# Performance work log

Hardware: AMD Instinct MI355X
Metric: run time of the kernel (lower is better)

Reference implementation:

```python
import jax, jax.numpy as jnp
import numpy as np

N_VERTS = 100000
N_JOINTS = 24
N_BETAS = 10
N_POSEDIRS = 207  # (24-1)*9
# Standard SMPL kinematic tree parents
PARENTS = np.array([-1, 0, 0, 0, 1, 2, 3, 4, 5, 6, 7, 8, 9, 9, 9, 12, 13, 14, 16, 17, 18, 19, 20, 21])


def setup_inputs() -> dict:
    key = jax.random.key(0)
    ks = jax.random.split(key, 9)
    f = jnp.float32
    return {
        "betas": jax.random.normal(ks[0], (N_BETAS,), f),
        "pose": jax.random.normal(ks[1], (N_JOINTS, 3), f) * 0.2,
        "scale": jnp.ones((1,), f),
        "trans": jax.random.normal(ks[2], (3,), f),
        "v_template": jax.random.normal(ks[3], (N_VERTS, 3), f),
        "shapedirs": jax.random.normal(ks[4], (N_VERTS, 3, N_BETAS), f) * 0.01,
        "posedirs": jax.random.normal(ks[5], (N_VERTS, 3, N_POSEDIRS), f) * 0.01,
        "J_regressor": jax.random.uniform(ks[6], (N_JOINTS, N_VERTS), f) / N_VERTS,
        "weights": jax.nn.softmax(jax.random.normal(ks[7], (N_VERTS, N_JOINTS), f), axis=-1),
    }


def rodrigues(r):
    """Axis-angle [J,3] -> rotation matrices [J,3,3] (matches torch impl; eps kept tiny+deterministic)."""
    theta = jnp.linalg.norm(r + 1e-8, axis=-1, keepdims=True)  # [J,1]
    r_hat = r / theta
    z = jnp.zeros_like(r_hat[:, 0])
    K = jnp.stack([z, -r_hat[:, 2], r_hat[:, 1],
                   r_hat[:, 2], z, -r_hat[:, 0],
                   -r_hat[:, 1], r_hat[:, 0], z], axis=1).reshape(-1, 3, 3)
    c = jnp.cos(theta)[..., None]  # [J,1,1]
    s = jnp.sin(theta)[..., None]
    outer = r_hat[:, :, None] * r_hat[:, None, :]  # [J,3,3]
    I = jnp.eye(3, dtype=r.dtype)
    return c * I + (1.0 - c) * outer + s * K


def reference(betas, pose, scale, trans, v_template, shapedirs, posedirs, J_regressor, weights):
    dt = v_template.dtype
    # blend shapes
    v_shaped = jnp.einsum('vks,s->vk', shapedirs, betas) + v_template  # [V,3]
    J = J_regressor @ v_shaped  # [24,3]
    R = rodrigues(pose)  # [24,3,3]
    I3 = jnp.eye(3, dtype=dt)
    lrotmin = (R[1:] - I3).reshape(-1)  # [207]
    v_posed = v_shaped + jnp.einsum('vkp,p->vk', posedirs, lrotmin)  # [V,3]
    # forward kinematics over 24-joint chain
    bottom = jnp.array([[0.0, 0.0, 0.0, 1.0]], dtype=dt)
    def make_A(Ri, t):
        return jnp.concatenate([jnp.concatenate([Ri, t[:, None]], axis=1), bottom], axis=0)  # [4,4]
    As = [make_A(R[0], J[0])]
    for i in range(1, N_JOINTS):
        p = int(PARENTS[i])
        As.append(As[p] @ make_A(R[i], J[i] - J[p]))
    G = jnp.stack(As)  # [24,4,4]
    # remove rest-pose joint locations
    Jh = jnp.concatenate([J, jnp.zeros((N_JOINTS, 1), dt)], axis=1)  # [24,4]
    corr = jnp.einsum('jab,jb->ja', G, Jh)  # [24,4]
    rel = G - jnp.concatenate([jnp.zeros((N_JOINTS, 4, 3), dt), corr[:, :, None]], axis=2)
    # linear blend skinning
    T = jnp.einsum('vj,jab->vab', weights, rel)  # [V,4,4]
    vh = jnp.concatenate([v_posed, jnp.ones((v_posed.shape[0], 1), dt)], axis=1)  # [V,4]
    v = jnp.einsum('vab,vb->va', T, vh)[:, :3]  # [V,3]
    return v * scale.reshape(()) + trans[None, :]
```

## Files before the change

kernel.cpp:

```cpp
#include <hip/hip_runtime.h>

#define NV 100000
#define NJ 24
#define NP 207
#define NPART 25
#define VPB 8
#define NTILES (NV / VPB)
#define TF4 1242
#define GRIDF 1024

__global__ __launch_bounds__(256) void k_shape(
    const float* __restrict__ betas, const float* __restrict__ v_template,
    const float* __restrict__ shapedirs, float* __restrict__ v_shaped) {
  __shared__ float sb[10];
  if (threadIdx.x < 10) sb[threadIdx.x] = betas[threadIdx.x];
  __syncthreads();
  int R = blockIdx.x * 256 + threadIdx.x;
  if (R >= 3 * NV) return;
  const float2* sd = (const float2*)(shapedirs + (size_t)R * 10);
  float a = v_template[R];
  #pragma unroll
  for (int s = 0; s < 5; ++s) {
    float2 x = sd[s];
    a += x.x * sb[2 * s] + x.y * sb[2 * s + 1];
  }
  v_shaped[R] = a;
}

__global__ __launch_bounds__(256) void k_jreg(
    const float* __restrict__ Jreg, const float* __restrict__ v_shaped,
    float* __restrict__ jpart) {
  int j = blockIdx.x, part = blockIdx.y, tid = threadIdx.x;
  const int SL = NV / NPART;
  int v0 = part * SL;
  const float4* w4 = (const float4*)(Jreg + (size_t)j * NV + v0);
  const float4* s4 = (const float4*)(v_shaped + (size_t)3 * v0);
  float s0 = 0.f, s1 = 0.f, s2 = 0.f;
  for (int i4 = tid; i4 < SL / 4; i4 += 256) {
    float4 w = w4[i4];
    float4 A = s4[3 * i4 + 0];
    float4 B = s4[3 * i4 + 1];
    float4 C = s4[3 * i4 + 2];
    s0 += w.x * A.x + w.y * A.w + w.z * B.z + w.w * C.y;
    s1 += w.x * A.y + w.y * B.x + w.z * B.w + w.w * C.z;
    s2 += w.x * A.z + w.y * B.y + w.z * C.x + w.w * C.w;
  }
  __shared__ float red[256][3];
  red[tid][0] = s0; red[tid][1] = s1; red[tid][2] = s2;
  __syncthreads();
  for (int off = 128; off > 0; off >>= 1) {
    if (tid < off) {
      red[tid][0] += red[tid + off][0];
      red[tid][1] += red[tid + off][1];
      red[tid][2] += red[tid + off][2];
    }
    __syncthreads();
  }
  if (tid < 3) jpart[(part * NJ + j) * 3 + tid] = red[0][tid];
}

__global__ __launch_bounds__(64) void k_fk(
    const float* __restrict__ pose, const float* __restrict__ jpart,
    float* __restrict__ lrot, float* __restrict__ rel) {
  __shared__ float J[NJ][3];
  __shared__ float R[NJ][9];
  __shared__ float G[NJ][12];
  int tid = threadIdx.x;
  if (tid < NJ) {
    for (int k = 0; k < 3; ++k) {
      float a = 0.f;
      for (int part = 0; part < NPART; ++part) a += jpart[(part * NJ + tid) * 3 + k];
      J[tid][k] = a;
    }
    float rx = pose[tid * 3 + 0], ry = pose[tid * 3 + 1], rz = pose[tid * 3 + 2];
    float tx = rx + 1e-8f, ty = ry + 1e-8f, tz = rz + 1e-8f;
    float theta = sqrtf(tx * tx + ty * ty + tz * tz);
    float x = rx / theta, y = ry / theta, z = rz / theta;
    float c = cosf(theta), s = sinf(theta), C = 1.f - c;
    float* Rr = R[tid];
    Rr[0] = c + C * x * x;     Rr[1] = C * x * y - s * z; Rr[2] = C * x * z + s * y;
    Rr[3] = C * x * y + s * z; Rr[4] = c + C * y * y;     Rr[5] = C * y * z - s * x;
    Rr[6] = C * x * z - s * y; Rr[7] = C * y * z + s * x; Rr[8] = c + C * z * z;
    if (tid >= 1) {
      #pragma unroll
      for (int e = 0; e < 9; ++e) {
        float id = (e == 0 || e == 4 || e == 8) ? 1.f : 0.f;
        lrot[(tid - 1) * 9 + e] = Rr[e] - id;
      }
    }
  }
  __syncthreads();
  if (tid == 0) {
    const int par[NJ] = {-1,0,0,0,1,2,3,4,5,6,7,8,9,9,9,12,13,14,16,17,18,19,20,21};
    for (int a = 0; a < 3; ++a) {
      for (int b = 0; b < 3; ++b) G[0][a * 4 + b] = R[0][a * 3 + b];
      G[0][a * 4 + 3] = J[0][a];
    }
    for (int i = 1; i < NJ; ++i) {
      int p = par[i];
      float t0 = J[i][0] - J[p][0], t1 = J[i][1] - J[p][1], t2 = J[i][2] - J[p][2];
      for (int a = 0; a < 3; ++a) {
        float g0 = G[p][a * 4 + 0], g1 = G[p][a * 4 + 1], g2 = G[p][a * 4 + 2];
        for (int b = 0; b < 3; ++b)
          G[i][a * 4 + b] = g0 * R[i][0 * 3 + b] + g1 * R[i][1 * 3 + b] + g2 * R[i][2 * 3 + b];
        G[i][a * 4 + 3] = G[p][a * 4 + 3] + g0 * t0 + g1 * t1 + g2 * t2;
      }
    }
  }
  __syncthreads();
  if (tid < NJ) {
    for (int a = 0; a < 3; ++a) {
      float corr = G[tid][a * 4 + 0] * J[tid][0] + G[tid][a * 4 + 1] * J[tid][1] +
                   G[tid][a * 4 + 2] * J[tid][2];
      rel[tid * 12 + a * 4 + 0] = G[tid][a * 4 + 0];
      rel[tid * 12 + a * 4 + 1] = G[tid][a * 4 + 1];
      rel[tid * 12 + a * 4 + 2] = G[tid][a * 4 + 2];
      rel[tid * 12 + a * 4 + 3] = G[tid][a * 4 + 3] - corr;
    }
  }
}

__device__ __forceinline__ void stage_tile(float4* dst, const float4* src, int tid) {
  #pragma unroll
  for (int r = 0; r < 5; ++r) {
    int i4 = r * 256 + tid;
    if (i4 < TF4) {
      __builtin_amdgcn_global_load_lds(
          (const __attribute__((address_space(1))) void*)(src + i4),
          (__attribute__((address_space(3))) void*)(dst + r * 256 + (tid & 192)),
          16, 0, 0);
    }
  }
}

__global__ __launch_bounds__(256, 4) void k_fused(
    const float* __restrict__ posedirs, const float* __restrict__ wgt,
    const float* __restrict__ lrot, const float* __restrict__ rel,
    const float* __restrict__ scale, const float* __restrict__ trans,
    float* __restrict__ vbuf) {
  __shared__ float4 tile[2][TF4];
  int tid = threadIdx.x, b = blockIdx.x;
  int wid = tid >> 6, lane = tid & 63, half = lane >> 5, lj = lane & 31;
  const float4* pd4 = (const float4*)posedirs;

  int vv0 = b * VPB + (wid << 1) + half;
  float pvl = (lj < 3) ? vbuf[(size_t)3 * vv0 + lj] : 0.f;
  float wj  = (lj < NJ) ? wgt[(size_t)vv0 * NJ + lj] : 0.f;
  __builtin_amdgcn_sched_barrier(0);
  stage_tile(&tile[0][0], pd4 + (size_t)b * TF4, tid);

  float llr[7];
  #pragma unroll
  for (int e = 0; e < 7; ++e) {
    int p = lj + 32 * e;
    llr[e] = (p < NP) ? lrot[p] : 0.f;
  }
  float rlq[12];
  #pragma unroll
  for (int e = 0; e < 12; ++e) rlq[e] = (lj < NJ) ? rel[lj * 12 + e] : 0.f;
  float sc = scale[0];
  float tr = (lj < 3) ? trans[lj] : 0.f;

  int nt = (NTILES - 1 - b) / GRIDF + 1;
  asm volatile("s_waitcnt vmcnt(5)" ::: "memory");
  __syncthreads();

  for (int it = 0; it < nt; ++it) {
    int cur = it & 1;
    int tnE = b + (it + 1) * GRIDF;
    if (tnE >= NTILES) tnE = NTILES - 1;
    int vvn = tnE * VPB + (wid << 1) + half;
    float pvl_n = (lj < 3) ? vbuf[(size_t)3 * vvn + lj] : 0.f;
    float wj_n  = (lj < NJ) ? wgt[(size_t)vvn * NJ + lj] : 0.f;
    __builtin_amdgcn_sched_barrier(0);
    stage_tile(&tile[cur ^ 1][0], pd4 + (size_t)tnE * TF4, tid);
    asm volatile("s_waitcnt vmcnt(7)" ::: "memory");
    __builtin_amdgcn_sched_barrier(0);
    __builtin_amdgcn_s_barrier();
    __builtin_amdgcn_sched_barrier(0);

    int vv = (b + it * GRIDF) * VPB + (wid << 1) + half;
    const float* row = (const float*)&tile[cur][0] + ((wid << 1) + half) * (3 * NP);
    float a0 = 0.f, a1 = 0.f, a2 = 0.f;
    #pragma unroll
    for (int e = 0; e < 7; ++e) {
      int p = lj + 32 * e;
      if (p < NP) {
        float l = llr[e];
        a0 += row[p] * l;
        a1 += row[NP + p] * l;
        a2 += row[2 * NP + p] * l;
      }
    }
    #pragma unroll
    for (int off = 16; off > 0; off >>= 1) {
      a0 += __shfl_xor(a0, off);
      a1 += __shfl_xor(a1, off);
      a2 += __shfl_xor(a2, off);
    }
    int gb = lane & 32;
    float p0 = __shfl(pvl, gb + 0) + a0;
    float p1 = __shfl(pvl, gb + 1) + a1;
    float p2 = __shfl(pvl, gb + 2) + a2;
    float q0 = rlq[0] * p0 + rlq[1] * p1 + rlq[2]  * p2 + rlq[3];
    float q1 = rlq[4] * p0 + rlq[5] * p1 + rlq[6]  * p2 + rlq[7];
    float q2 = rlq[8] * p0 + rlq[9] * p1 + rlq[10] * p2 + rlq[11];
    float r0 = wj * q0, r1 = wj * q1, r2 = wj * q2;
    #pragma unroll
    for (int off = 16; off > 0; off >>= 1) {
      r0 += __shfl_xor(r0, off);
      r1 += __shfl_xor(r1, off);
      r2 += __shfl_xor(r2, off);
    }
    if (lj < 3) {
      float oo = (lj == 0) ? r0 : (lj == 1) ? r1 : r2;
      vbuf[(size_t)3 * vv + lj] = oo * sc + tr;
    }
    __builtin_amdgcn_sched_barrier(0);
    __builtin_amdgcn_s_barrier();
    __builtin_amdgcn_sched_barrier(0);

    pvl = pvl_n; wj = wj_n;
  }
  asm volatile("s_waitcnt vmcnt(0)" ::: "memory");
}

extern "C" void kernel_launch(void* const* d_in, const int* in_sizes, int n_in,
                              void* d_out, int out_size, void* d_ws, size_t ws_size,
                              hipStream_t stream) {
  const float* betas      = (const float*)d_in[0];
  const float* pose       = (const float*)d_in[1];
  const float* scale      = (const float*)d_in[2];
  const float* trans      = (const float*)d_in[3];
  const float* v_template = (const float*)d_in[4];
  const float* shapedirs  = (const float*)d_in[5];
  const float* posedirs   = (const float*)d_in[6];
  const float* Jreg       = (const float*)d_in[7];
  const float* weights    = (const float*)d_in[8];
  float* out = (float*)d_out;
  float* ws  = (float*)d_ws;

  float* jpart = ws;
  float* lrot  = ws + 1800;
  float* rel   = ws + 2048;

  k_shape<<<(3 * NV + 255) / 256, 256, 0, stream>>>(betas, v_template, shapedirs, out);
  k_jreg<<<dim3(NJ, NPART), 256, 0, stream>>>(Jreg, out, jpart);
  k_fk<<<1, 64, 0, stream>>>(pose, jpart, lrot, rel);
  k_fused<<<GRIDF, 256, 0, stream>>>(posedirs, weights, lrot, rel, scale, trans, out);
}
```

Baseline: 67.47 us.

## Fold forward-kinematics kernel into fused skinning kernel and widen shape-blend loads

Removes the single-block k_fk launch: every block of the fused kernel now reduces the transposed joint partials, computes Rodrigues rotations, runs the kinematic chain (parallelized over 3 rows) and builds rel/lrot in the spare second LDS tile buffer. This overlaps the first posedirs tile prefetch and cuts a serial launch plus a global round-trip. In exchange every block repeats the tiny FK computation redundantly. k_shape now handles two rows per thread with float4 loads to widen memory accesses.

```diff
diff --git a/kernel.cpp b/kernel.cpp
--- a/kernel.cpp
+++ b/kernel.cpp
@@ -15,21 +15,25 @@
   __shared__ float sb[10];
   if (threadIdx.x < 10) sb[threadIdx.x] = betas[threadIdx.x];
   __syncthreads();
-  int R = blockIdx.x * 256 + threadIdx.x;
-  if (R >= 3 * NV) return;
-  const float2* sd = (const float2*)(shapedirs + (size_t)R * 10);
-  float a = v_template[R];
-  #pragma unroll
-  for (int s = 0; s < 5; ++s) {
-    float2 x = sd[s];
-    a += x.x * sb[2 * s] + x.y * sb[2 * s + 1];
-  }
-  v_shaped[R] = a;
+  int t = blockIdx.x * 256 + threadIdx.x;
+  if (t >= 3 * NV / 2) return;
+  const float4* sd4 = (const float4*)(shapedirs + (size_t)t * 20);
+  float4 f0 = sd4[0], f1 = sd4[1], f2 = sd4[2], f3 = sd4[3], f4v = sd4[4];
+  float2 vt = ((const float2*)v_template)[t];
+  float a = vt.x
+          + f0.x * sb[0] + f0.y * sb[1] + f0.z * sb[2] + f0.w * sb[3]
+          + f1.x * sb[4] + f1.y * sb[5] + f1.z * sb[6] + f1.w * sb[7]
+          + f2.x * sb[8] + f2.y * sb[9];
+  float b = vt.y
+          + f2.z * sb[0] + f2.w * sb[1]
+          + f3.x * sb[2] + f3.y * sb[3] + f3.z * sb[4] + f3.w * sb[5]
+          + f4v.x * sb[6] + f4v.y * sb[7] + f4v.z * sb[8] + f4v.w * sb[9];
+  ((float2*)v_shaped)[t] = make_float2(a, b);
 }
 
 __global__ __launch_bounds__(256) void k_jreg(
     const float* __restrict__ Jreg, const float* __restrict__ v_shaped,
-    float* __restrict__ jpart) {
+    float* __restrict__ jpT) {
   int j = blockIdx.x, part = blockIdx.y, tid = threadIdx.x;
   const int SL = NV / NPART;
   int v0 = part * SL;
@@ -56,68 +60,7 @@
     }
     __syncthreads();
   }
-  if (tid < 3) jpart[(part * NJ + j) * 3 + tid] = red[0][tid];
-}
-
-__global__ __launch_bounds__(64) void k_fk(
-    const float* __restrict__ pose, const float* __restrict__ jpart,
-    float* __restrict__ lrot, float* __restrict__ rel) {
-  __shared__ float J[NJ][3];
-  __shared__ float R[NJ][9];
-  __shared__ float G[NJ][12];
-  int tid = threadIdx.x;
-  if (tid < NJ) {
-    for (int k = 0; k < 3; ++k) {
-      float a = 0.f;
-      for (int part = 0; part < NPART; ++part) a += jpart[(part * NJ + tid) * 3 + k];
-      J[tid][k] = a;
-    }
-    float rx = pose[tid * 3 + 0], ry = pose[tid * 3 + 1], rz = pose[tid * 3 + 2];
-    float tx = rx + 1e-8f, ty = ry + 1e-8f, tz = rz + 1e-8f;
-    float theta = sqrtf(tx * tx + ty * ty + tz * tz);
-    float x = rx / theta, y = ry / theta, z = rz / theta;
-    float c = cosf(theta), s = sinf(theta), C = 1.f - c;
-    float* Rr = R[tid];
-    Rr[0] = c + C * x * x;     Rr[1] = C * x * y - s * z; Rr[2] = C * x * z + s * y;
-    Rr[3] = C * x * y + s * z; Rr[4] = c + C * y * y;     Rr[5] = C * y * z - s * x;
-    Rr[6] = C * x * z - s * y; Rr[7] = C * y * z + s * x; Rr[8] = c + C * z * z;
-    if (tid >= 1) {
-      #pragma unroll
-      for (int e = 0; e < 9; ++e) {
-        float id = (e == 0 || e == 4 || e == 8) ? 1.f : 0.f;
-        lrot[(tid - 1) * 9 + e] = Rr[e] - id;
-      }
-    }
-  }
-  __syncthreads();
-  if (tid == 0) {
-    const int par[NJ] = {-1,0,0,0,1,2,3,4,5,6,7,8,9,9,9,12,13,14,16,17,18,19,20,21};
-    for (int a = 0; a < 3; ++a) {
-      for (int b = 0; b < 3; ++b) G[0][a * 4 + b] = R[0][a * 3 + b];
-      G[0][a * 4 + 3] = J[0][a];
-    }
-    for (int i = 1; i < NJ; ++i) {
-      int p = par[i];
-      float t0 = J[i][0] - J[p][0], t1 = J[i][1] - J[p][1], t2 = J[i][2] - J[p][2];
-      for (int a = 0; a < 3; ++a) {
-        float g0 = G[p][a * 4 + 0], g1 = G[p][a * 4 + 1], g2 = G[p][a * 4 + 2];
-        for (int b = 0; b < 3; ++b)
-          G[i][a * 4 + b] = g0 * R[i][0 * 3 + b] + g1 * R[i][1 * 3 + b] + g2 * R[i][2 * 3 + b];
-        G[i][a * 4 + 3] = G[p][a * 4 + 3] + g0 * t0 + g1 * t1 + g2 * t2;
-      }
-    }
-  }
-  __syncthreads();
-  if (tid < NJ) {
-    for (int a = 0; a < 3; ++a) {
-      float corr = G[tid][a * 4 + 0] * J[tid][0] + G[tid][a * 4 + 1] * J[tid][1] +
-                   G[tid][a * 4 + 2] * J[tid][2];
-      rel[tid * 12 + a * 4 + 0] = G[tid][a * 4 + 0];
-      rel[tid * 12 + a * 4 + 1] = G[tid][a * 4 + 1];
-      rel[tid * 12 + a * 4 + 2] = G[tid][a * 4 + 2];
-      rel[tid * 12 + a * 4 + 3] = G[tid][a * 4 + 3] - corr;
-    }
-  }
+  if (tid < 3) jpT[(j * 3 + tid) * 32 + part] = red[0][tid];
 }
 
 __device__ __forceinline__ void stage_tile(float4* dst, const float4* src, int tid) {
@@ -135,7 +78,7 @@
 
 __global__ __launch_bounds__(256, 4) void k_fused(
     const float* __restrict__ posedirs, const float* __restrict__ wgt,
-    const float* __restrict__ lrot, const float* __restrict__ rel,
+    const float* __restrict__ pose, const float* __restrict__ jpT,
     const float* __restrict__ scale, const float* __restrict__ trans,
     float* __restrict__ vbuf) {
   __shared__ float4 tile[2][TF4];
@@ -149,20 +92,88 @@
   __builtin_amdgcn_sched_barrier(0);
   stage_tile(&tile[0][0], pd4 + (size_t)b * TF4, tid);
 
+  float* fkJ  = (float*)&tile[1][0];
+  float* fkR  = fkJ + 72;
+  float* fkG  = fkJ + 288;
+  float* lrs  = fkJ + 576;
+  float* relS = fkJ + 784;
+  if (tid < NJ * 3) {
+    const float* src = jpT + tid * 32;
+    float a = 0.f;
+    #pragma unroll
+    for (int i = 0; i < NPART; ++i) a += src[i];
+    fkJ[tid] = a;
+  }
+  if (tid < NJ) {
+    float rx = pose[tid * 3 + 0], ry = pose[tid * 3 + 1], rz = pose[tid * 3 + 2];
+    float tx = rx + 1e-8f, ty = ry + 1e-8f, tz = rz + 1e-8f;
+    float theta = sqrtf(tx * tx + ty * ty + tz * tz);
+    float x = rx / theta, y = ry / theta, z = rz / theta;
+    float c = cosf(theta), s = sinf(theta), C = 1.f - c;
+    float Rr[9];
+    Rr[0] = c + C * x * x;     Rr[1] = C * x * y - s * z; Rr[2] = C * x * z + s * y;
+    Rr[3] = C * x * y + s * z; Rr[4] = c + C * y * y;     Rr[5] = C * y * z - s * x;
+    Rr[6] = C * x * z - s * y; Rr[7] = C * y * z + s * x; Rr[8] = c + C * z * z;
+    #pragma unroll
+    for (int e = 0; e < 9; ++e) fkR[tid * 9 + e] = Rr[e];
+    if (tid >= 1) {
+      #pragma unroll
+      for (int e = 0; e < 9; ++e) {
+        float id = (e == 0 || e == 4 || e == 8) ? 1.f : 0.f;
+        lrs[(tid - 1) * 9 + e] = Rr[e] - id;
+      }
+    }
+  }
+  __syncthreads();
+  if (tid < 3) {
+    const int par[NJ] = {-1,0,0,0,1,2,3,4,5,6,7,8,9,9,9,12,13,14,16,17,18,19,20,21};
+    int a = tid;
+    fkG[a * 4 + 0] = fkR[a * 3 + 0];
+    fkG[a * 4 + 1] = fkR[a * 3 + 1];
+    fkG[a * 4 + 2] = fkR[a * 3 + 2];
+    fkG[a * 4 + 3] = fkJ[a];
+    #pragma unroll
+    for (int i = 1; i < NJ; ++i) {
+      int p = par[i];
+      float t0 = fkJ[i * 3 + 0] - fkJ[p * 3 + 0];
+      float t1 = fkJ[i * 3 + 1] - fkJ[p * 3 + 1];
+      float t2 = fkJ[i * 3 + 2] - fkJ[p * 3 + 2];
+      float g0 = fkG[p * 12 + a * 4 + 0], g1 = fkG[p * 12 + a * 4 + 1];
+      float g2 = fkG[p * 12 + a * 4 + 2], g3 = fkG[p * 12 + a * 4 + 3];
+      fkG[i * 12 + a * 4 + 0] = g0 * fkR[i * 9 + 0] + g1 * fkR[i * 9 + 3] + g2 * fkR[i * 9 + 6];
+      fkG[i * 12 + a * 4 + 1] = g0 * fkR[i * 9 + 1] + g1 * fkR[i * 9 + 4] + g2 * fkR[i * 9 + 7];
+      fkG[i * 12 + a * 4 + 2] = g0 * fkR[i * 9 + 2] + g1 * fkR[i * 9 + 5] + g2 * fkR[i * 9 + 8];
+      fkG[i * 12 + a * 4 + 3] = g3 + g0 * t0 + g1 * t1 + g2 * t2;
+    }
+  }
+  __syncthreads();
+  if (tid < NJ) {
+    #pragma unroll
+    for (int a = 0; a < 3; ++a) {
+      float corr = fkG[tid * 12 + a * 4 + 0] * fkJ[tid * 3 + 0] +
+                   fkG[tid * 12 + a * 4 + 1] * fkJ[tid * 3 + 1] +
+                   fkG[tid * 12 + a * 4 + 2] * fkJ[tid * 3 + 2];
+      relS[tid * 12 + a * 4 + 0] = fkG[tid * 12 + a * 4 + 0];
+      relS[tid * 12 + a * 4 + 1] = fkG[tid * 12 + a * 4 + 1];
+      relS[tid * 12 + a * 4 + 2] = fkG[tid * 12 + a * 4 + 2];
+      relS[tid * 12 + a * 4 + 3] = fkG[tid * 12 + a * 4 + 3] - corr;
+    }
+  }
+  __syncthreads();
+
   float llr[7];
   #pragma unroll
   for (int e = 0; e < 7; ++e) {
     int p = lj + 32 * e;
-    llr[e] = (p < NP) ? lrot[p] : 0.f;
+    llr[e] = (p < NP) ? lrs[p] : 0.f;
   }
   float rlq[12];
   #pragma unroll
-  for (int e = 0; e < 12; ++e) rlq[e] = (lj < NJ) ? rel[lj * 12 + e] : 0.f;
+  for (int e = 0; e < 12; ++e) rlq[e] = (lj < NJ) ? relS[lj * 12 + e] : 0.f;
   float sc = scale[0];
   float tr = (lj < 3) ? trans[lj] : 0.f;
 
   int nt = (NTILES - 1 - b) / GRIDF + 1;
-  asm volatile("s_waitcnt vmcnt(5)" ::: "memory");
   __syncthreads();
 
   for (int it = 0; it < nt; ++it) {
@@ -240,12 +251,9 @@
   float* out = (float*)d_out;
   float* ws  = (float*)d_ws;
 
-  float* jpart = ws;
-  float* lrot  = ws + 1800;
-  float* rel   = ws + 2048;
-
-  k_shape<<<(3 * NV + 255) / 256, 256, 0, stream>>>(betas, v_template, shapedirs, out);
-  k_jreg<<<dim3(NJ, NPART), 256, 0, stream>>>(Jreg, out, jpart);
-  k_fk<<<1, 64, 0, stream>>>(pose, jpart, lrot, rel);
-  k_fused<<<GRIDF, 256, 0, stream>>>(posedirs, weights, lrot, rel, scale, trans, out);
-}
+  float* jpT = ws;
+
+  k_shape<<<(3 * NV / 2 + 255) / 256, 256, 0, stream>>>(betas, v_template, shapedirs, out);
+  k_jreg<<<dim3(NJ, NPART), 256, 0, stream>>>(Jreg, out, jpT);
+  k_fused<<<GRIDF, 256, 0, stream>>>(posedirs, weights, pose, jpT, scale, trans, out);
+}
```

Result: faster. 61.62 us (-8.7%).
